# Optimization experiments

Measured on AMD Instinct MI355X. Metric: run time of the kernel, lower is better.

## Reference

```python
import jax, jax.numpy as jnp
import numpy as np

EPS = 1e-5
KEEP_FRAC = 0.925


def conv1x1(x, w, b):
    # x: [B,C,H,W], w: [O,C], b: [O]
    return jnp.einsum('bchw,oc->bohw', x, w) + b[None, :, None, None]


def adain_norm(x):
    m = x.mean(axis=(2, 3), keepdims=True)
    v = x.var(axis=(2, 3), keepdims=True)
    return (x - m) / jnp.sqrt(v + EPS)


def zca_norm(x):
    B, C, H, W = x.shape
    f = x.reshape(B, C, H * W)
    m = f.mean(axis=-1, keepdims=True)
    fc = f - m
    cov = jnp.einsum('bcn,bdn->bcd', fc, fc) / (H * W - 1) + EPS * jnp.eye(C, dtype=x.dtype)
    s, U = jnp.linalg.eigh(cov)
    Ud = U * (1.0 / jnp.sqrt(s + EPS))[:, None, :]          # U @ diag(s^-1/2)
    whiten = jnp.einsum('bce,bde->bcd', Ud, U)              # U diag U^T
    out = jnp.einsum('bcd,bdn->bcn', whiten, fc)
    return out.reshape(B, C, H, W)


def correlation_block(xq, yk, wf, bf, wg, bg):
    B, C, H, W = xq.shape
    f = conv1x1(xq, wf, bf).reshape(B, C, -1)   # [B,C,n_x]
    g = conv1x1(yk, wg, bg).reshape(B, C, -1)   # [B,C,n_y]
    energy = jnp.einsum('bcn,bcm->bnm', f, g)   # f^T g : [B,n_x,n_y]
    corr = jax.nn.softmax(energy, axis=-1)
    atten = corr.mean(axis=1, keepdims=True)    # mean over n_x -> [B,1,n_y]
    return corr, atten


def attn_mask(a):
    # a: [B,1,n]; zero the positions of the k smallest values (union over batch, as in torch)
    n = a.shape[2]
    k = int(n * KEEP_FRAC)
    idx = jnp.argsort(a, axis=2)[:, :, :k]                   # smallest k per (b, channel)
    mask = jnp.ones_like(a).at[:, :, idx.reshape(-1)].set(0.0)
    return mask


def corr_mask(mx, my):
    # mx: [B,1,n_x], my: [B,1,n_y] -> equality mask [B,n_x,n_y]
    return (mx[:, 0, :, None] == my[:, 0, None, :]).astype(mx.dtype)


def savanet_forward(x, y, f_w, f_b, g_w, g_b, sa_f_w, sa_f_b, sa_g_w, sa_g_b, h_w, h_b, out_w, out_b):
    B, C, H, W = x.shape
    n = H * W
    x_adain = adain_norm(x)
    y_adain = adain_norm(y)
    x_zca = zca_norm(x)
    y_zca = zca_norm(y)
    correlation, _ = correlation_block(x_adain, y_adain, f_w, f_b, g_w, g_b)
    _, atten_x = correlation_block(x_zca, x_zca, sa_f_w, sa_f_b, sa_g_w, sa_g_b)
    _, atten_y = correlation_block(y_zca, y_zca, sa_f_w, sa_f_b, sa_g_w, sa_g_b)
    mx = attn_mask(atten_x)
    my = attn_mask(atten_y)
    cmask = corr_mask(mx, my)                               # [B,n,n]
    correlation = cmask * correlation
    l1 = jnp.clip(jnp.abs(correlation).sum(axis=2, keepdims=True), 1e-12, None)
    correlation = correlation / l1                          # F.normalize(p=1, dim=2)
    h = conv1x1(y, h_w, h_b).reshape(B, C, n)               # [B,C,n_y]
    residual = jnp.einsum('bcm,bnm->bcn', h, correlation)   # h @ corr^T -> [B,C,n_x]
    residual = residual.reshape(B, C, H, W)
    residual = conv1x1(residual, out_w, out_b)
    output = x + residual
    return output, atten_x, atten_y


def setup_inputs() -> dict:
    key = jax.random.key(0)
    ks = jax.random.split(key, 10)
    B, C, H, W = 2, 512, 64, 64
    scale = 0.02
    d = {
        'x': jax.random.normal(ks[0], (B, C, H, W), dtype=jnp.float32),
        'y': jax.random.normal(ks[1], (B, C, H, W), dtype=jnp.float32),
        'f_w': jax.random.normal(ks[2], (C, C), dtype=jnp.float32) * scale,
        'f_b': jnp.zeros((C,), dtype=jnp.float32),
        'g_w': jax.random.normal(ks[3], (C, C), dtype=jnp.float32) * scale,
        'g_b': jnp.zeros((C,), dtype=jnp.float32),
        'sa_f_w': jax.random.normal(ks[4], (C, C), dtype=jnp.float32) * scale,
        'sa_f_b': jnp.zeros((C,), dtype=jnp.float32),
        'sa_g_w': jax.random.normal(ks[5], (C, C), dtype=jnp.float32) * scale,
        'sa_g_b': jnp.zeros((C,), dtype=jnp.float32),
        'h_w': jax.random.normal(ks[6], (C, C), dtype=jnp.float32) * scale,
        'h_b': jnp.zeros((C,), dtype=jnp.float32),
        'out_w': jax.random.normal(ks[7], (C, C), dtype=jnp.float32) * scale,
        'out_b': jnp.zeros((C,), dtype=jnp.float32),
    }
    return d


def reference(x, y, f_w, f_b, g_w, g_b, sa_f_w, sa_f_b, sa_g_w, sa_g_b, h_w, h_b, out_w, out_b):
    return savanet_forward(x, y, f_w, f_b, g_w, g_b, sa_f_w, sa_f_b, sa_g_w, sa_g_b, h_w, h_b, out_w, out_b)
```

## Files before the change

### kernel.cpp

```cpp
#include <hip/hip_runtime.h>
#include <cstdint>

static constexpr int B2 = 2;
static constexpr int C = 512;
static constexpr int N = 4096;
static constexpr long CN = (long)C * N;
static constexpr long NC = (long)N * C;
static constexpr long CC = (long)C * C;
static constexpr long NN = (long)N * N;
static constexpr float EPSC = 1e-5f;
static constexpr int KSEL = 308;
static constexpr int NS_ITERS = 4;

typedef __attribute__((ext_vector_type(8))) __bf16 bf16x8;
typedef __attribute__((ext_vector_type(4))) float f32x4;

__device__ __forceinline__ float wredSum(float v){
#pragma unroll
  for (int o = 32; o >= 1; o >>= 1) v += __shfl_xor(v, o, 64);
  return v;
}

__device__ __forceinline__ void gld16(const __bf16* g, __bf16* l){
  __builtin_amdgcn_global_load_lds(
      (const __attribute__((address_space(1))) void*)g,
      (__attribute__((address_space(3))) void*)l, 16, 0, 0);
}

__device__ __forceinline__ void splitw(float v, __bf16* ph, __bf16* pl, long o){
  __bf16 h = (__bf16)v;
  ph[o] = h;
  pl[o] = (__bf16)(v - (float)h);
}

template<int PASSES, int TMH, int OUTMODE, int ROWP>
__global__ __launch_bounds__(256) void k_mm(
    const __bf16* __restrict__ Ah, const __bf16* __restrict__ Al,
    const __bf16* __restrict__ Bh, const __bf16* __restrict__ Bl,
    float* __restrict__ Cf, __bf16* __restrict__ Coh, __bf16* __restrict__ Col,
    int Nn, int K, long sAz, long sBz, long sCz,
    float alpha, const float* __restrict__ alpha_ptr,
    const float* __restrict__ brow, long sBr,
    const float* __restrict__ bcol, long sBc,
    const float* __restrict__ c0p,
    const float* __restrict__ addsrc, long sAddz,
    float* __restrict__ Pm, float* __restrict__ Ps)
{
  constexpr int NB = (PASSES == 3) ? 4 : 2;
  constexpr int SB = (PASSES == 3) ? 2 : 1;
  __shared__ __align__(16) __bf16 sm[NB][128 * 32];
  __shared__ float pmx[2][128], psx[2][128];
  const int z = blockIdx.z;
  const int nwx = gridDim.x;
  int lin = blockIdx.y * nwx + blockIdx.x;
  const int nwg = nwx * gridDim.y;
  if ((nwg & 7) == 0){
    const int cpx = nwg >> 3;
    lin = (lin & 7) * cpx + (lin >> 3);
  }
  const int i0 = (lin % nwx) * 128;
  const int j0 = (lin / nwx) * 128;
  const int tid = threadIdx.x;
  const int lane = tid & 63;
  const int w = tid >> 6;
  const int wr = (w >> 1) * 64, wc = (w & 1) * 64;
  const int lr = lane & 15;
  const int g = lane >> 4;

  const __bf16* pAh = Ah + (long)z * sAz + (long)i0 * K;
  const __bf16* pBh = Bh + (long)z * sBz + (long)j0 * K;
  const __bf16* pAl = (PASSES == 3) ? (Al + (long)z * sAz + (long)i0 * K) : nullptr;
  const __bf16* pBl = (PASSES == 3) ? (Bl + (long)z * sBz + (long)j0 * K) : nullptr;

  f32x4 acc[4][4] = {};

  for (int kt = 0; kt < K; kt += 32){
#pragma unroll
    for (int p = 0; p < 2; ++p){
      const int t2 = p * 256 + tid;
      const int row = t2 >> 2;
      const int gs = (t2 & 3) ^ ((row >> 1) & 3);
      const long go = (long)row * K + kt + gs * 8;
      gld16(pAh + go, &sm[0][t2 * 8]);
      gld16(pBh + go, &sm[SB][t2 * 8]);
      if constexpr (PASSES == 3){
        gld16(pAl + go, &sm[1][t2 * 8]);
        gld16(pBl + go, &sm[3][t2 * 8]);
      }
    }
    __syncthreads();
    bf16x8 fa[4], fal[4], fb[4], fbl[4];
#pragma unroll
    for (int mi = 0; mi < 4; ++mi){
      const int row = wr + mi * 16 + lr;
      const int off = row * 32 + ((g ^ ((row >> 1) & 3)) * 8);
      fa[mi] = *(const bf16x8*)(&sm[0][off]);
      if constexpr (PASSES == 3) fal[mi] = *(const bf16x8*)(&sm[1][off]);
    }
#pragma unroll
    for (int ni = 0; ni < 4; ++ni){
      const int row = wc + ni * 16 + lr;
      const int off = row * 32 + ((g ^ ((row >> 1) & 3)) * 8);
      fb[ni] = *(const bf16x8*)(&sm[SB][off]);
      if constexpr (PASSES == 3) fbl[ni] = *(const bf16x8*)(&sm[3][off]);
    }
#pragma unroll
    for (int mi = 0; mi < 4; ++mi)
#pragma unroll
      for (int ni = 0; ni < 4; ++ni){
        acc[mi][ni] = __builtin_amdgcn_mfma_f32_16x16x32_bf16(fa[mi], fb[ni], acc[mi][ni], 0, 0, 0);
        if constexpr (PASSES == 3){
          acc[mi][ni] = __builtin_amdgcn_mfma_f32_16x16x32_bf16(fa[mi],  fbl[ni], acc[mi][ni], 0, 0, 0);
          acc[mi][ni] = __builtin_amdgcn_mfma_f32_16x16x32_bf16(fal[mi], fb[ni],  acc[mi][ni], 0, 0, 0);
        }
      }
    __syncthreads();
  }

  float al2 = alpha;
  if (alpha_ptr) al2 *= alpha_ptr[z];
  const float c0v = c0p ? c0p[z] : 0.f;
#pragma unroll
  for (int mi = 0; mi < 4; ++mi){
    float mrow[4] = {-3.4e38f, -3.4e38f, -3.4e38f, -3.4e38f};
    float srow[4] = {0.f, 0.f, 0.f, 0.f};
#pragma unroll
    for (int ni = 0; ni < 4; ++ni){
      const int col = j0 + wc + ni * 16 + lr;
      const float bc = (bcol ? bcol[z * sBc + col] : 0.f) + c0v;
#pragma unroll
      for (int j = 0; j < 4; ++j){
        const int row = i0 + wr + mi * 16 + g * 4 + j;
        float v = acc[mi][ni][j] * al2;
        if (TMH) v = (((row == col) ? 3.f : 0.f) - v) * 0.5f;
        if (brow) v += brow[z * sBr + row];
        v += bc;
        if (addsrc) v += addsrc[(long)z * sAddz + (long)row * Nn + col];
        const long o = (long)z * sCz + (long)row * Nn + col;
        if (OUTMODE == 0){ Cf[o] = v; }
        else if (OUTMODE == 1){ __bf16 h = (__bf16)v; Coh[o] = h; Col[o] = (__bf16)(v - (float)h); }
        else { Coh[o] = (__bf16)v; }
        if constexpr (ROWP){
          if (v > mrow[j]){ srow[j] *= __expf(mrow[j] - v); mrow[j] = v; }
          srow[j] += __expf(v - mrow[j]);
        }
      }
    }
    if constexpr (ROWP){
#pragma unroll
      for (int j = 0; j < 4; ++j){
        float m = mrow[j], s = srow[j];
#pragma unroll
        for (int o = 1; o <= 8; o <<= 1){
          const float mo = __shfl_xor(m, o, 64);
          const float so = __shfl_xor(s, o, 64);
          const float nm = fmaxf(m, mo);
          s = s * __expf(m - nm) + so * __expf(mo - nm);
          m = nm;
        }
        if (lr == 0){
          const int rl = wr + mi * 16 + g * 4 + j;
          pmx[w & 1][rl] = m;
          psx[w & 1][rl] = s;
        }
      }
    }
  }
  if constexpr (ROWP){
    __syncthreads();
    if (tid < 128){
      const float m0 = pmx[0][tid], s0 = psx[0][tid];
      const float m1 = pmx[1][tid], s1 = psx[1][tid];
      const float nm = fmaxf(m0, m1);
      const float s = s0 * __expf(m0 - nm) + s1 * __expf(m1 - nm);
      Pm[(long)(j0 >> 7) * N + i0 + tid] = nm;
      Ps[(long)(j0 >> 7) * N + i0 + tid] = s;
    }
  }
}

template<int TMH, int OUTMODE, int NSYZ>
__global__ __launch_bounds__(256) void k_mm64(
    const __bf16* __restrict__ Ah, const __bf16* __restrict__ Al,
    const __bf16* __restrict__ Bh, const __bf16* __restrict__ Bl,
    const __bf16* __restrict__ tH, const __bf16* __restrict__ tL,
    float* __restrict__ Cf, __bf16* __restrict__ Coh, __bf16* __restrict__ Col,
    int Nn, int K, long sAz, long sBz, long sCz, float alpha)
{
  __shared__ __align__(16) __bf16 sm[4][64 * 64];
  const int z = blockIdx.z;
  const __bf16 *bAh, *bAl, *bBh, *bBl;
  long oC;
  if constexpr (NSYZ){
    if (z < 4){
      bAh = Ah + (long)z * CC; bAl = Al + (long)z * CC;
      bBh = tH + (long)z * CC; bBl = tL + (long)z * CC;
      oC = (long)z * CC;
    } else {
      const int zz = z - 4;
      bAh = tH + (long)zz * CC; bAl = tL + (long)zz * CC;
      bBh = Ah + (long)(4 + zz) * CC; bBl = Al + (long)(4 + zz) * CC;
      oC = (long)(4 + zz) * CC;
    }
  } else {
    bAh = Ah + (long)z * sAz; bAl = Al + (long)z * sAz;
    bBh = Bh + (long)z * sBz; bBl = Bl + (long)z * sBz;
    oC = (long)z * sCz;
  }
  const int i0 = blockIdx.x * 64;
  const int j0 = blockIdx.y * 64;
  const int tid = threadIdx.x;
  const int lane = tid & 63;
  const int w = tid >> 6;
  const int wr = (w >> 1) * 32, wc = (w & 1) * 32;
  const int lr = lane & 15;
  const int g = lane >> 4;

  const __bf16* pAh = bAh + (long)i0 * K;
  const __bf16* pAl = bAl + (long)i0 * K;
  const __bf16* pBh = bBh + (long)j0 * K;
  const __bf16* pBl = bBl + (long)j0 * K;

  f32x4 acc[2][2] = {};

  for (int kt = 0; kt < K; kt += 64){
#pragma unroll
    for (int p = 0; p < 2; ++p){
      const int t2 = p * 256 + tid;
      const int row = t2 >> 3;
      const int gs = (t2 & 7) ^ (row & 7);
      const long go = (long)row * K + kt + gs * 8;
      gld16(pAh + go, &sm[0][t2 * 8]);
      gld16(pAl + go, &sm[1][t2 * 8]);
      gld16(pBh + go, &sm[2][t2 * 8]);
      gld16(pBl + go, &sm[3][t2 * 8]);
    }
    __syncthreads();
#pragma unroll
    for (int ks = 0; ks < 2; ++ks){
      bf16x8 fa[2], fal[2], fb[2], fbl[2];
#pragma unroll
      for (int mi = 0; mi < 2; ++mi){
        const int row = wr + mi * 16 + lr;
        const int off = row * 64 + (((ks * 4 + g) ^ (row & 7)) * 8);
        fa[mi]  = *(const bf16x8*)(&sm[0][off]);
        fal[mi] = *(const bf16x8*)(&sm[1][off]);
      }
#pragma unroll
      for (int ni = 0; ni < 2; ++ni){
        const int row = wc + ni * 16 + lr;
        const int off = row * 64 + (((ks * 4 + g) ^ (row & 7)) * 8);
        fb[ni]  = *(const bf16x8*)(&sm[2][off]);
        fbl[ni] = *(const bf16x8*)(&sm[3][off]);
      }
#pragma unroll
      for (int mi = 0; mi < 2; ++mi)
#pragma unroll
        for (int ni = 0; ni < 2; ++ni){
          acc[mi][ni] = __builtin_amdgcn_mfma_f32_16x16x32_bf16(fa[mi],  fb[ni],  acc[mi][ni], 0, 0, 0);
          acc[mi][ni] = __builtin_amdgcn_mfma_f32_16x16x32_bf16(fa[mi],  fbl[ni], acc[mi][ni], 0, 0, 0);
          acc[mi][ni] = __builtin_amdgcn_mfma_f32_16x16x32_bf16(fal[mi], fb[ni],  acc[mi][ni], 0, 0, 0);
        }
    }
    __syncthreads();
  }

#pragma unroll
  for (int mi = 0; mi < 2; ++mi){
#pragma unroll
    for (int ni = 0; ni < 2; ++ni){
      const int col = j0 + wc + ni * 16 + lr;
#pragma unroll
      for (int j = 0; j < 4; ++j){
        const int row = i0 + wr + mi * 16 + g * 4 + j;
        float v = acc[mi][ni][j] * alpha;
        if (TMH) v = (((row == col) ? 3.f : 0.f) - v) * 0.5f;
        const long o = oC + (long)row * Nn + col;
        if (OUTMODE == 0){ Cf[o] = v; }
        else { __bf16 h = (__bf16)v; Coh[o] = h; Col[o] = (__bf16)(v - (float)h); }
      }
    }
  }
}

__global__ __launch_bounds__(256) void k_pv(
    const __bf16* __restrict__ E, const __bf16* __restrict__ Bh,
    const float* __restrict__ rm, const float* __restrict__ rsc,
    const float* __restrict__ mxv, const float* __restrict__ myv,
    __bf16* __restrict__ resH)
{
  __shared__ __align__(16) __bf16 sa[64 * 64];
  __shared__ __align__(16) __bf16 sb[128 * 64];
  const int z = blockIdx.z;
  int lin = blockIdx.y * 64 + blockIdx.x;
  lin = (lin & 7) * 32 + (lin >> 3);
  const int n0 = (lin & 63) * 64;
  const int c0 = (lin >> 6) * 128;
  const int tid = threadIdx.x;
  const int lane = tid & 63;
  const int w = tid >> 6;
  const int wr = (w >> 1) * 32, wc = (w & 1) * 64;
  const int lr = lane & 15, g = lane >> 4;

  const __bf16* pe = E + (long)z * NN + (long)n0 * N;
  const __bf16* pB = Bh + (long)z * CN + (long)c0 * N;

  const int ar = tid >> 2;
  const int slot = tid & 3;
  const float rmv = rm[(long)z * N + n0 + ar];
  const float rsv = rsc[(long)z * N + n0 + ar];
  const float tgt = mxv[n0 + ar];
  const __bf16* per = pe + (long)ar * N;

  f32x4 acc[2][4] = {};

  for (int kt = 0; kt < N; kt += 64){
#pragma unroll
    for (int d = 0; d < 2; ++d){
      const int gd = slot * 2 + d;
      const bf16x8 ev = *(const bf16x8*)(per + kt + gd * 8);
      const float4 m0 = *(const float4*)(myv + kt + gd * 8);
      const float4 m1 = *(const float4*)(myv + kt + gd * 8 + 4);
      bf16x8 pk;
      pk[0] = (__bf16)((m0.x == tgt) ? __expf((float)ev[0] - rmv) * rsv : 0.f);
      pk[1] = (__bf16)((m0.y == tgt) ? __expf((float)ev[1] - rmv) * rsv : 0.f);
      pk[2] = (__bf16)((m0.z == tgt) ? __expf((float)ev[2] - rmv) * rsv : 0.f);
      pk[3] = (__bf16)((m0.w == tgt) ? __expf((float)ev[3] - rmv) * rsv : 0.f);
      pk[4] = (__bf16)((m1.x == tgt) ? __expf((float)ev[4] - rmv) * rsv : 0.f);
      pk[5] = (__bf16)((m1.y == tgt) ? __expf((float)ev[5] - rmv) * rsv : 0.f);
      pk[6] = (__bf16)((m1.z == tgt) ? __expf((float)ev[6] - rmv) * rsv : 0.f);
      pk[7] = (__bf16)((m1.w == tgt) ? __expf((float)ev[7] - rmv) * rsv : 0.f);
      *(bf16x8*)(&sa[ar * 64 + ((gd ^ (ar & 7)) * 8)]) = pk;
    }
#pragma unroll
    for (int p = 0; p < 4; ++p){
      const int t2 = p * 256 + tid;
      const int row = t2 >> 3;
      const int gs = (t2 & 7) ^ (row & 7);
      gld16(pB + (long)row * N + kt + gs * 8, &sb[t2 * 8]);
    }
    __syncthreads();
#pragma unroll
    for (int ks = 0; ks < 2; ++ks){
      bf16x8 fa[2], fb[4];
#pragma unroll
      for (int mi = 0; mi < 2; ++mi){
        const int row = wr + mi * 16 + lr;
        fa[mi] = *(const bf16x8*)(&sa[row * 64 + (((ks * 4 + g) ^ (row & 7)) * 8)]);
      }
#pragma unroll
      for (int ni = 0; ni < 4; ++ni){
        const int row = wc + ni * 16 + lr;
        fb[ni] = *(const bf16x8*)(&sb[row * 64 + (((ks * 4 + g) ^ (row & 7)) * 8)]);
      }
#pragma unroll
      for (int mi = 0; mi < 2; ++mi)
#pragma unroll
        for (int ni = 0; ni < 4; ++ni)
          acc[mi][ni] = __builtin_amdgcn_mfma_f32_16x16x32_bf16(fa[mi], fb[ni], acc[mi][ni], 0, 0, 0);
    }
    __syncthreads();
  }
#pragma unroll
  for (int mi = 0; mi < 2; ++mi)
#pragma unroll
    for (int ni = 0; ni < 4; ++ni){
      const int c = c0 + wc + ni * 16 + lr;
#pragma unroll
      for (int j = 0; j < 4; ++j){
        const int n = n0 + wr + mi * 16 + g * 4 + j;
        resH[(long)z * NC + (long)n * C + c] = (__bf16)acc[mi][ni][j];
      }
    }
}

__global__ __launch_bounds__(256) void k_wtw(const float* __restrict__ A, const float* __restrict__ B,
                                             float* __restrict__ C2, float alpha){
  __shared__ float sa[16][32], sb[16][32];
  const int i0 = blockIdx.x * 32, j0 = blockIdx.y * 32;
  const int t = threadIdx.x;
  const int ti = t & 15, tj = t >> 4;
  const int li = t & 31, lc = t >> 5;
  float acc[2][2] = {};
  for (int cb = 0; cb < C; cb += 16){
    sa[lc][li]     = A[(long)(cb + lc) * C + i0 + li];
    sa[lc + 8][li] = A[(long)(cb + lc + 8) * C + i0 + li];
    sb[lc][li]     = B[(long)(cb + lc) * C + j0 + li];
    sb[lc + 8][li] = B[(long)(cb + lc + 8) * C + j0 + li];
    __syncthreads();
#pragma unroll
    for (int c = 0; c < 16; ++c){
      const float a0 = sa[c][ti * 2], a1 = sa[c][ti * 2 + 1];
      const float b0 = sb[c][tj * 2], b1 = sb[c][tj * 2 + 1];
      acc[0][0] = fmaf(a0, b0, acc[0][0]); acc[0][1] = fmaf(a0, b1, acc[0][1]);
      acc[1][0] = fmaf(a1, b0, acc[1][0]); acc[1][1] = fmaf(a1, b1, acc[1][1]);
    }
    __syncthreads();
  }
#pragma unroll
  for (int r = 0; r < 2; ++r)
#pragma unroll
    for (int s = 0; s < 2; ++s)
      C2[(long)(i0 + ti * 2 + r) * C + j0 + tj * 2 + s] = acc[r][s] * alpha;
}

__global__ __launch_bounds__(256) void k_wtv(const float* __restrict__ W, const float* __restrict__ b,
                                             float* __restrict__ u){
  __shared__ float sb2[C];
  const int t = threadIdx.x;
  sb2[t] = b[t]; sb2[t + 256] = b[t + 256];
  __syncthreads();
  const int e = blockIdx.x * 256 + t;
  float acc = 0.f;
  for (int c = 0; c < C; ++c) acc = fmaf(W[(long)c * C + e], sb2[c], acc);
  u[e] = acc;
}

__global__ void k_dot2(const float* __restrict__ a1, const float* __restrict__ b1,
                       const float* __restrict__ a2, const float* __restrict__ b2,
                       float* __restrict__ c0m2, float* __restrict__ c0s4){
  const int t = threadIdx.x;
  float s1 = 0.f, s2 = 0.f;
  for (int i = t; i < C; i += 256){ s1 += a1[i] * b1[i]; s2 += a2[i] * b2[i]; }
  __shared__ float sh1[4], sh2[4];
  s1 = wredSum(s1); s2 = wredSum(s2);
  if ((t & 63) == 0){ sh1[t >> 6] = s1; sh2[t >> 6] = s2; }
  __syncthreads();
  if (t == 0){
    float d1 = sh1[0] + sh1[1] + sh1[2] + sh1[3];
    float d2 = sh2[0] + sh2[1] + sh2[2] + sh2[3];
    c0m2[0] = d1; c0m2[1] = d1;
    c0s4[0] = d2; c0s4[1] = d2; c0s4[2] = d2; c0s4[3] = d2;
  }
}

__global__ __launch_bounds__(256) void k_pixvec(const __bf16* __restrict__ X, const float* __restrict__ u,
                                                float* __restrict__ out){
  const int z = blockIdx.y;
  const int wv = threadIdx.x >> 6, lane = threadIdx.x & 63;
  const int n = blockIdx.x * 4 + wv;
  float acc = 0.f;
  for (int d = lane; d < C; d += 64) acc += (float)X[(long)z * NC + (long)n * C + d] * u[d];
  acc = wredSum(acc);
  if (lane == 0) out[(long)z * N + n] = acc;
}

__global__ __launch_bounds__(256) void k_stats(const float* __restrict__ x, const float* __restrict__ y,
                                               float* __restrict__ meanv, float* __restrict__ invs){
  const int bid = blockIdx.x;
  const int t = bid >> 9, c = bid & 511;
  const float* src = (t < 2 ? x : y) + (long)(t & 1) * CN + (long)c * N;
  const int tid = threadIdx.x;
  float s1 = 0.f, s2 = 0.f;
  for (int i = tid; i < N; i += 256){ float v = src[i]; s1 += v; s2 += v * v; }
  __shared__ float sh1[4], sh2[4];
  s1 = wredSum(s1); s2 = wredSum(s2);
  if ((tid & 63) == 0){ sh1[tid >> 6] = s1; sh2[tid >> 6] = s2; }
  __syncthreads();
  if (tid == 0){
    float m = (sh1[0] + sh1[1] + sh1[2] + sh1[3]) * (1.f / (float)N);
    float ex2 = (sh2[0] + sh2[1] + sh2[2] + sh2[3]) * (1.f / (float)N);
    float var = ex2 - m * m;
    meanv[t * C + c] = m;
    invs[t * C + c] = rsqrtf((var > 0.f ? var : 0.f) + EPSC);
  }
}

__global__ __launch_bounds__(256) void k_prep(const float* __restrict__ src,
                                              const float* __restrict__ meanv, const float* __restrict__ invs, int toff,
                                              __bf16* __restrict__ adH,
                                              __bf16* __restrict__ fcH, __bf16* __restrict__ fcL,
                                              __bf16* __restrict__ ccH, __bf16* __restrict__ ccL,
                                              __bf16* __restrict__ rwH){
  __shared__ float tile[64][65];
  const int z = blockIdx.z;
  const int n0 = blockIdx.x * 64;
  const int c0 = blockIdx.y * 64;
  const int tid = threadIdx.x;
  const int tx = tid & 63, ty = tid >> 6;
  const int tgt = toff + z;
#pragma unroll
  for (int it = 0; it < 16; ++it){
    const int cc = it * 4 + ty;
    const float v = src[(long)z * CN + (long)(c0 + cc) * N + n0 + tx];
    tile[cc][tx] = v;
    const float cen = v - meanv[tgt * C + c0 + cc];
    splitw(cen, ccH, ccL, (long)tgt * CN + (long)(c0 + cc) * N + n0 + tx);
  }
  __syncthreads();
  const float m = meanv[tgt * C + c0 + tx];
  const float r = invs[tgt * C + c0 + tx];
#pragma unroll
  for (int it = 0; it < 16; ++it){
    const int p = it * 4 + ty;
    const float v = tile[tx][p];
    const float cen = v - m;
    const long o = (long)z * NC + (long)(n0 + p) * C + c0 + tx;
    adH[o] = (__bf16)(cen * r);
    splitw(cen, fcH, fcL, (long)tgt * NC + (long)(n0 + p) * C + c0 + tx);
    if (rwH) rwH[o] = (__bf16)v;
  }
}

__global__ __launch_bounds__(256) void k_wcvt(const float* __restrict__ s, __bf16* __restrict__ h,
                                              __bf16* __restrict__ l, int n){
  int i = blockIdx.x * 256 + threadIdx.x;
  if (i < n) splitw(s[i], h, l, i);
}
__global__ __launch_bounds__(256) void k_wcvt_h(const float* __restrict__ s, __bf16* __restrict__ h, int n){
  int i = blockIdx.x * 256 + threadIdx.x;
  if (i < n) h[i] = (__bf16)s[i];
}

__global__ void k_diag(float* __restrict__ cov){
  const int z = blockIdx.x, t = threadIdx.x;
  for (int i = t; i < C; i += 256) cov[(long)z * CC + (long)i * C + i] += 2.f * EPSC;
}

__global__ __launch_bounds__(256) void k_powit(const float* __restrict__ cov,
                                               float* __restrict__ invt, float* __restrict__ invsqt){
  __shared__ float v[C], red[4];
  const int z = blockIdx.x, t = threadIdx.x;
  const float* A = cov + (long)z * CC;
  const int j0 = t, j1 = t + 256;
  v[j0] = 1.f + 0.0003f * (float)j0;
  v[j1] = 1.f + 0.0003f * (float)j1;
  __syncthreads();
  float lam = 1.f;
  for (int it = 0; it < 4; ++it){
    float w0a = 0.f, w0b = 0.f, w1a = 0.f, w1b = 0.f;
#pragma unroll 8
    for (int c = 0; c < C; c += 2){
      const float vc0 = v[c], vc1 = v[c + 1];
      w0a = fmaf(A[(long)c * C + j0], vc0, w0a);
      w1a = fmaf(A[(long)c * C + j1], vc0, w1a);
      w0b = fmaf(A[(long)(c + 1) * C + j0], vc1, w0b);
      w1b = fmaf(A[(long)(c + 1) * C + j1], vc1, w1b);
    }
    const float w0 = w0a + w0b, w1 = w1a + w1b;
    float s = w0 * w0 + w1 * w1;
    s = wredSum(s);
    if ((t & 63) == 0) red[t >> 6] = s;
    __syncthreads();
    const float nrm = sqrtf(red[0] + red[1] + red[2] + red[3]);
    lam = nrm;
    const float inv = 1.f / nrm;
    v[j0] = w0 * inv;
    v[j1] = w1 * inv;
    __syncthreads();
  }
  if (t == 0){
    const float tt = 1.02f * lam;
    invt[z] = 1.f / tt;
    invsqt[z] = rsqrtf(tt);
  }
}

__global__ __launch_bounds__(256) void k_ns_init(const float* __restrict__ cov, const float* __restrict__ invt,
                                                 __bf16* __restrict__ h, __bf16* __restrict__ l,
                                                 __bf16* __restrict__ cph, __bf16* __restrict__ cpl){
  const int r = blockIdx.x, z = blockIdx.y;
  const long base = (long)z * CC + (long)r * C;
  const float it = invt[z];
  for (int i = threadIdx.x; i < C; i += 256){
    const float v = cov[base + i] * it;
    splitw(v, h, l, base + i);
    splitw(v, cph, cpl, base + i);
    h[4 * CC + base + i] = (__bf16)((i == r) ? 1.f : 0.f);
    l[4 * CC + base + i] = (__bf16)0.f;
  }
}

__global__ __launch_bounds__(256) void k_prowmerge(const float* __restrict__ Pm, const float* __restrict__ Ps,
                                                   float* __restrict__ rm, float* __restrict__ rsc){
  const int row = blockIdx.x * 256 + threadIdx.x;
  float m = -3.4e38f, s = 0.f;
#pragma unroll 4
  for (int p = 0; p < 32; ++p){
    const float mp = Pm[(long)p * N + row];
    const float sp = Ps[(long)p * N + row];
    const float nm = fmaxf(m, mp);
    s = s * __expf(m - nm) + sp * __expf(mp - nm);
    m = nm;
  }
  rm[row] = m;
  rsc[row] = 1.f / s;
}

__global__ __launch_bounds__(256) void k_colaccum(const float* __restrict__ E, const float* __restrict__ rowmax,
                                                  const float* __restrict__ rowscale, float* __restrict__ partials){
  const int j = (blockIdx.x * 256 + threadIdx.x) * 4;
  const int r0 = blockIdx.y * 128;
  float4 acc = {0.f, 0.f, 0.f, 0.f};
  for (int r2 = r0; r2 < r0 + 128; ++r2){
    const float4 e = *reinterpret_cast<const float4*>(E + (long)r2 * N + j);
    const float rmv = rowmax[r2], rsv = rowscale[r2];
    acc.x += __expf(e.x - rmv) * rsv;
    acc.y += __expf(e.y - rmv) * rsv;
    acc.z += __expf(e.z - rmv) * rsv;
    acc.w += __expf(e.w - rmv) * rsv;
  }
  *reinterpret_cast<float4*>(partials + (long)blockIdx.y * N + j) = acc;
}

__global__ __launch_bounds__(256) void k_colreduce(const float* __restrict__ partials, float* __restrict__ att){
  const int j = blockIdx.x * 256 + threadIdx.x;
  float s = 0.f;
#pragma unroll 4
  for (int p = 0; p < 32; ++p) s += partials[(long)p * N + j];
  att[j] = s * (1.f / (float)N);
}

__global__ __launch_bounds__(256) void k_rowstats1(
    const __bf16* __restrict__ E, const float* __restrict__ mx, const float* __restrict__ my,
    float* __restrict__ rowmax, float* __restrict__ rowscale)
{
  const int zz = blockIdx.y;
  const int r0 = blockIdx.x * 16;
  const int tid = threadIdx.x;
  const int rr = tid >> 4;
  const int l16 = tid & 15;
  const int row = r0 + rr;
  const __bf16* pe = E + (long)zz * NN + (long)row * N;
  const float target = mx[row];
  float m = -3.4e38f, s = 0.f, sm = 0.f;
  for (int i = l16 * 8; i < N; i += 128){
    const bf16x8 ev = *(const bf16x8*)(pe + i);
    const float4 w0 = *(const float4*)(my + i);
    const float4 w1 = *(const float4*)(my + i + 4);
    float e[8];
#pragma unroll
    for (int k = 0; k < 8; ++k) e[k] = (float)ev[k];
    float mv = fmaxf(fmaxf(fmaxf(e[0], e[1]), fmaxf(e[2], e[3])),
                     fmaxf(fmaxf(e[4], e[5]), fmaxf(e[6], e[7])));
    if (mv > m){ const float sc = __expf(m - mv); s *= sc; sm *= sc; m = mv; }
    float x0 = __expf(e[0] - m), x1 = __expf(e[1] - m), x2 = __expf(e[2] - m), x3 = __expf(e[3] - m);
    float x4 = __expf(e[4] - m), x5 = __expf(e[5] - m), x6 = __expf(e[6] - m), x7 = __expf(e[7] - m);
    s += ((x0 + x1) + (x2 + x3)) + ((x4 + x5) + (x6 + x7));
    if (w0.x == target) sm += x0;
    if (w0.y == target) sm += x1;
    if (w0.z == target) sm += x2;
    if (w0.w == target) sm += x3;
    if (w1.x == target) sm += x4;
    if (w1.y == target) sm += x5;
    if (w1.z == target) sm += x6;
    if (w1.w == target) sm += x7;
  }
#pragma unroll
  for (int o = 8; o >= 1; o >>= 1){
    const float mo = __shfl_xor(m, o, 64);
    const float so = __shfl_xor(s, o, 64);
    const float smo = __shfl_xor(sm, o, 64);
    const float nm = fmaxf(m, mo);
    const float sc0 = __expf(m - nm), sc1 = __expf(mo - nm);
    s = s * sc0 + so * sc1;
    sm = sm * sc0 + smo * sc1;
    m = nm;
  }
  if (l16 == 0){
    float l1 = sm / s;
    if (l1 < 1e-12f) l1 = 1e-12f;
    rowscale[(long)zz * N + row] = 1.f / (s * l1);
    rowmax[(long)zz * N + row] = m;
  }
}

__global__ __launch_bounds__(256) void k_radix(const float* __restrict__ a, float* __restrict__ thr){
  __shared__ unsigned int vals[N];
  __shared__ float shc[4];
  __shared__ unsigned int p_sh;
  __shared__ int k_sh;
  const float* pa = a + (long)blockIdx.x * N;
  const int tid = threadIdx.x;
  for (int i = tid; i < N; i += 256) vals[i] = __float_as_uint(pa[i]);
  if (tid == 0){ p_sh = 0u; k_sh = KSEL; }
  __syncthreads();
  for (int b = 31; b >= 0; --b){
    const unsigned int bit = 1u << b;
    const unsigned int above = (b == 31) ? 0u : ~((bit << 1) - 1u);
    const unsigned int p = p_sh;
    int cnt = 0;
    for (int i = tid; i < N; i += 256){
      unsigned int v = vals[i];
      if ((v & above) == p && (v & bit)) cnt++;
    }
    float cf = wredSum((float)cnt);
    if ((tid & 63) == 0) shc[tid >> 6] = cf;
    __syncthreads();
    if (tid == 0){
      int c1 = (int)(shc[0] + shc[1] + shc[2] + shc[3] + 0.5f);
      if (k_sh <= c1) p_sh = p | bit;
      else k_sh -= c1;
    }
    __syncthreads();
  }
  if (tid == 0) thr[blockIdx.x] = __uint_as_float(p_sh);
}

__global__ __launch_bounds__(256) void k_mask(const float* __restrict__ ax, const float* __restrict__ ay,
                                              const float* __restrict__ thr, float* __restrict__ mx,
                                              float* __restrict__ my){
  int j = blockIdx.x * 256 + threadIdx.x;
  mx[j] = (ax[j] >= thr[0] && ax[N + j] >= thr[1]) ? 1.f : 0.f;
  my[j] = (ay[j] >= thr[2] && ay[N + j] >= thr[3]) ? 1.f : 0.f;
}

extern "C" void kernel_launch(void* const* d_in, const int* in_sizes, int n_in,
                              void* d_out, int out_size, void* d_ws, size_t ws_size,
                              hipStream_t stream)
{
  const float* x     = (const float*)d_in[0];
  const float* y     = (const float*)d_in[1];
  const float* f_w   = (const float*)d_in[2];
  const float* f_b   = (const float*)d_in[3];
  const float* g_w   = (const float*)d_in[4];
  const float* g_b   = (const float*)d_in[5];
  const float* saf_w = (const float*)d_in[6];
  const float* saf_b = (const float*)d_in[7];
  const float* sag_w = (const float*)d_in[8];
  const float* sag_b = (const float*)d_in[9];
  const float* h_w   = (const float*)d_in[10];
  const float* h_b   = (const float*)d_in[11];
  const float* ow    = (const float*)d_in[12];
  const float* ob    = (const float*)d_in[13];

  const size_t MBy = 1ull << 20;
  char* base = (char*)d_ws;
  if (ws_size < 206 * MBy) return;
  auto F  = [&](size_t off){ return (float*)(base + off); };
  auto Bp = [&](size_t off){ return (__bf16*)(base + off); };

  float *E0 = F(0);
  __bf16 *Ebf = Bp(0);
  __bf16 *ccH = Bp(0), *ccL = Bp(16*MBy);
  float  *covb = F(32*MBy);
  __bf16 *zpolH = Bp(36*MBy), *zpolL = Bp(38*MBy);
  __bf16 *covPH = Bp(40*MBy), *covPL = Bp(42*MBy);
  float  *KsTf = F(44*MBy), *K2tf = F(45*MBy);
  __bf16 *KsTH = Bp(46*MBy), *KsTL = Bp(46*MBy + 512*1024);
  __bf16 *K2tH = Bp(47*MBy), *hwH = Bp(47*MBy + 512*1024);
  __bf16 *tpH = Bp(48*MBy), *tpL = Bp(50*MBy);
  __bf16 *xaH = Bp(64*MBy);
  __bf16 *xzH = Bp(64*MBy), *xzL = Bp(80*MBy);
  __bf16 *ypmH = Bp(96*MBy);
  __bf16 *AsH = Bp(96*MBy), *AsL = Bp(112*MBy);
  __bf16 *fcH = Bp(128*MBy), *fcL = Bp(144*MBy);
  __bf16 *resH = Bp(128*MBy);
  __bf16 *nsAh = Bp(160*MBy), *nsAl = Bp(164*MBy);
  __bf16 *nsBh = Bp(168*MBy), *nsBl = Bp(172*MBy);
  __bf16 *A2H = Bp(176*MBy);
  __bf16 *yaH = Bp(184*MBy);
  __bf16 *hH  = Bp(192*MBy);
  __bf16 *owH = Bp(200*MBy);
  size_t so = 200 * MBy + 512 * 1024;
  auto SF = [&](size_t bytes){ float* p = F(so); so += bytes; return p; };
  float *meanv = SF(8*1024), *invs = SF(8*1024);
  float *rm = SF(32*1024), *rsc = SF(32*1024);
  float *mxv = SF(16*1024), *myv = SF(16*1024);
  float *rvec2 = SF(32*1024), *cvec2 = SF(32*1024);
  float *rvS = SF(64*1024), *cvS = SF(64*1024);
  float *u1m = SF(2*1024), *u2m = SF(2*1024), *u1s = SF(2*1024), *u2s = SF(2*1024);
  float *c0m2 = SF(64), *c0s4 = SF(64), *thr = SF(64);
  float *invt = SF(64), *invsqt = SF(64);
  float *partials = F(201*MBy);
  float *Pm = F(201*MBy + 512*1024);
  float *Ps = F(201*MBy + 1024*1024);

  float* outm = (float*)d_out;
  float* attx = outm + B2 * CN;
  float* atty = attx + (long)B2 * N;

  k_stats<<<dim3(4 * C), dim3(256), 0, stream>>>(x, y, meanv, invs);
  k_prep<<<dim3(64, 8, 2), dim3(256), 0, stream>>>(x, meanv, invs, 0, xaH, fcH, fcL, ccH, ccL, nullptr);
  k_prep<<<dim3(64, 8, 2), dim3(256), 0, stream>>>(y, meanv, invs, 2, yaH, fcH, fcL, ccH, ccL, ypmH);

  k_wtw<<<dim3(16, 16), dim3(256), 0, stream>>>(sag_w, saf_w, KsTf, 1.f);
  k_wtw<<<dim3(16, 16), dim3(256), 0, stream>>>(g_w, f_w, K2tf, 1.f);
  {
    const int nb = (int)(CC / 256);
    k_wcvt<<<nb, 256, 0, stream>>>(KsTf, KsTH, KsTL, (int)CC);
    k_wcvt_h<<<nb, 256, 0, stream>>>(K2tf, K2tH, (int)CC);
    k_wcvt_h<<<nb, 256, 0, stream>>>(h_w, hwH, (int)CC);
    k_wcvt_h<<<nb, 256, 0, stream>>>(ow, owH, (int)CC);
  }
  k_wtv<<<dim3(2), dim3(256), 0, stream>>>(g_w, f_b, u1m);
  k_wtv<<<dim3(2), dim3(256), 0, stream>>>(f_w, g_b, u2m);
  k_wtv<<<dim3(2), dim3(256), 0, stream>>>(sag_w, saf_b, u1s);
  k_wtv<<<dim3(2), dim3(256), 0, stream>>>(saf_w, sag_b, u2s);
  k_dot2<<<dim3(1), dim3(256), 0, stream>>>(f_b, g_b, saf_b, sag_b, c0m2, c0s4);
  k_pixvec<<<dim3(N / 4, 2), dim3(256), 0, stream>>>(xaH, u2m, rvec2);
  k_pixvec<<<dim3(N / 4, 2), dim3(256), 0, stream>>>(yaH, u1m, cvec2);

  k_mm64<0,0,0><<<dim3(8, 8, 4), dim3(256), 0, stream>>>(
      ccH, ccL, ccH, ccL, nullptr, nullptr, covb, nullptr, nullptr, C, N, CN, CN, CC, 1.f / (float)(N - 1));
  k_diag<<<dim3(4), dim3(256), 0, stream>>>(covb);
  k_powit<<<dim3(4), dim3(256), 0, stream>>>(covb, invt, invsqt);

  k_mm<1,0,2,0><<<dim3(32, 4, 2), dim3(256), 0, stream>>>(xaH, nullptr, K2tH, nullptr, nullptr, A2H, nullptr,
      C, C, NC, 0, NC, 1.f, nullptr, nullptr, 0, nullptr, 0, nullptr, nullptr, 0, nullptr, nullptr);
  k_mm<1,0,2,0><<<dim3(4, 32, 2), dim3(256), 0, stream>>>(hwH, nullptr, ypmH, nullptr, nullptr, hH, nullptr,
      N, C, 0, NC, CN, 1.f, nullptr, h_b, 0, nullptr, 0, nullptr, nullptr, 0, nullptr, nullptr);

  k_ns_init<<<dim3(C, 4), dim3(256), 0, stream>>>(covb, invt, nsAh, nsAl, covPH, covPL);
  __bf16 *cah = nsAh, *cal = nsAl, *cbh = nsBh, *cbl = nsBl;
  for (int it = 0; it < NS_ITERS; ++it){
    k_mm64<1,1,0><<<dim3(8, 8, 4), dim3(256), 0, stream>>>(
        cah + 4*CC, cal + 4*CC, cah, cal, nullptr, nullptr, nullptr, tpH, tpL, C, C, CC, CC, CC, 1.f);
    k_mm64<0,1,1><<<dim3(8, 8, 8), dim3(256), 0, stream>>>(
        cah, cal, nullptr, nullptr, tpH, tpL, nullptr, cbh, cbl, C, C, CC, CC, CC, 1.f);
    __bf16* t;
    t = cah; cah = cbh; cbh = t;
    t = cal; cal = cbl; cbl = t;
  }
  k_mm64<0,1,0><<<dim3(8, 8, 4), dim3(256), 0, stream>>>(
      cah + 4*CC, cal + 4*CC, cah + 4*CC, cal + 4*CC, nullptr, nullptr, nullptr, tpH, tpL, C, C, CC, CC, CC, 1.f);
  k_mm64<1,1,0><<<dim3(8, 8, 4), dim3(256), 0, stream>>>(
      covPH, covPL, tpH, tpL, nullptr, nullptr, nullptr, cbh, cbl, C, C, CC, CC, CC, 1.f);
  k_mm64<0,1,0><<<dim3(8, 8, 4), dim3(256), 0, stream>>>(
      cah + 4*CC, cal + 4*CC, cbh, cbl, nullptr, nullptr, nullptr, zpolH, zpolL, C, C, CC, CC, CC, 1.f);

  k_mm<3,0,1,0><<<dim3(32, 4, 4), dim3(256), 0, stream>>>(fcH, fcL, zpolH, zpolL, nullptr, xzH, xzL,
      C, C, NC, CC, NC, 1.f, invsqt, nullptr, 0, nullptr, 0, nullptr, nullptr, 0, nullptr, nullptr);

  k_pixvec<<<dim3(N / 4, 4), dim3(256), 0, stream>>>(xzH, u2s, rvS);
  k_pixvec<<<dim3(N / 4, 4), dim3(256), 0, stream>>>(xzH, u1s, cvS);
  k_mm<3,0,1,0><<<dim3(32, 4, 4), dim3(256), 0, stream>>>(xzH, xzL, KsTH, KsTL, nullptr, AsH, AsL,
      C, C, NC, 0, NC, 1.f, nullptr, nullptr, 0, nullptr, 0, nullptr, nullptr, 0, nullptr, nullptr);

  for (int z = 0; z < 4; ++z){
    k_mm<3,0,0,1><<<dim3(32, 32, 1), dim3(256), 0, stream>>>(AsH + (long)z*NC, AsL + (long)z*NC,
        xzH + (long)z*NC, xzL + (long)z*NC, E0, nullptr, nullptr,
        N, C, 0, 0, 0, 1.f, nullptr, rvS + (long)z*N, 0, cvS + (long)z*N, 0, c0s4, nullptr, 0, Pm, Ps);
    k_prowmerge<<<dim3(16), dim3(256), 0, stream>>>(Pm, Ps, rm, rsc);
    k_colaccum<<<dim3(4, 32), dim3(256), 0, stream>>>(E0, rm, rsc, partials);
    k_colreduce<<<dim3(16), dim3(256), 0, stream>>>(partials, (z < 2 ? attx : atty) + (long)(z & 1) * N);
  }

  k_radix<<<dim3(2), dim3(256), 0, stream>>>(attx, thr);
  k_radix<<<dim3(2), dim3(256), 0, stream>>>(atty, thr + 2);
  k_mask<<<dim3(16), dim3(256), 0, stream>>>(attx, atty, thr, mxv, myv);

  k_mm<1,0,2,0><<<dim3(32, 32, 2), dim3(256), 0, stream>>>(A2H, nullptr, yaH, nullptr, nullptr, Ebf, nullptr,
      N, C, NC, NC, NN, 1.f, nullptr, rvec2, N, cvec2, N, c0m2, nullptr, 0, nullptr, nullptr);
  k_rowstats1<<<dim3(N / 16, 2), dim3(256), 0, stream>>>(Ebf, mxv, myv, rm, rsc);
  k_pv<<<dim3(64, 4, 2), dim3(256), 0, stream>>>(Ebf, hH, rm, rsc, mxv, myv, resH);
  k_mm<1,0,0,0><<<dim3(4, 32, 2), dim3(256), 0, stream>>>(owH, nullptr, resH, nullptr, outm, nullptr, nullptr,
      N, C, 0, NC, CN, 1.f, nullptr, ob, 0, nullptr, 0, nullptr, x, CN, nullptr, nullptr);
}
```

Measured before the change: 1.272 ms.

## Replace 3-pass split-bf16 GEMMs with single-pass K=1536 concatenated hi/lo layout

Stores the zca-whitened activations, the self-attention weight and the projected activations in a concatenated [hi|lo|hi] or [hi|hi|lo] layout along K (width 1536). The 3-pass split-precision matmuls then become single-pass bf16 GEMMs over K=1536, and a leading-dimension parameter is added to the GEMM output. This is meant to remove the multi-pass B-tile loading and bookkeeping in the big N×N energy GEMMs while keeping the three cross terms. The cost is a larger workspace footprint, more bytes read per K, and a workspace layout that had to be reshuffled.

```diff
diff --git a/kernel.cpp b/kernel.cpp
--- a/kernel.cpp
+++ b/kernel.cpp
@@ -8,6 +8,7 @@
 static constexpr long NC = (long)N * C;
 static constexpr long CC = (long)C * C;
 static constexpr long NN = (long)N * N;
+static constexpr long NL = (long)N * 1536;
 static constexpr float EPSC = 1e-5f;
 static constexpr int KSEL = 308;
 static constexpr int NS_ITERS = 4;
@@ -38,7 +39,7 @@
     const __bf16* __restrict__ Ah, const __bf16* __restrict__ Al,
     const __bf16* __restrict__ Bh, const __bf16* __restrict__ Bl,
     float* __restrict__ Cf, __bf16* __restrict__ Coh, __bf16* __restrict__ Col,
-    int Nn, int K, long sAz, long sBz, long sCz,
+    int Nn, int K, int ldC, long sAz, long sBz, long sCz,
     float alpha, const float* __restrict__ alpha_ptr,
     const float* __restrict__ brow, long sBr,
     const float* __restrict__ bcol, long sBc,
@@ -136,10 +137,12 @@
         if (brow) v += brow[z * sBr + row];
         v += bc;
         if (addsrc) v += addsrc[(long)z * sAddz + (long)row * Nn + col];
-        const long o = (long)z * sCz + (long)row * Nn + col;
+        const long o = (long)z * sCz + (long)row * ldC + col;
         if (OUTMODE == 0){ Cf[o] = v; }
         else if (OUTMODE == 1){ __bf16 h = (__bf16)v; Coh[o] = h; Col[o] = (__bf16)(v - (float)h); }
-        else { Coh[o] = (__bf16)v; }
+        else if (OUTMODE == 2){ Coh[o] = (__bf16)v; }
+        else if (OUTMODE == 3){ __bf16 h = (__bf16)v; Coh[o] = h; Coh[o + 512] = (__bf16)(v - (float)h); Coh[o + 1024] = h; }
+        else { __bf16 h = (__bf16)v; Coh[o] = h; Coh[o + 512] = h; Coh[o + 1024] = (__bf16)(v - (float)h); }
         if constexpr (ROWP){
           if (v > mrow[j]){ srow[j] *= __expf(mrow[j] - v); mrow[j] = v; }
           srow[j] += __expf(v - mrow[j]);
@@ -435,12 +438,12 @@
 }
 
 __global__ __launch_bounds__(256) void k_pixvec(const __bf16* __restrict__ X, const float* __restrict__ u,
-                                                float* __restrict__ out){
+                                                float* __restrict__ out, long sz, int ld){
   const int z = blockIdx.y;
   const int wv = threadIdx.x >> 6, lane = threadIdx.x & 63;
   const int n = blockIdx.x * 4 + wv;
   float acc = 0.f;
-  for (int d = lane; d < C; d += 64) acc += (float)X[(long)z * NC + (long)n * C + d] * u[d];
+  for (int d = lane; d < C; d += 64) acc += (float)X[(long)z * sz + (long)n * ld + d] * u[d];
   acc = wredSum(acc);
   if (lane == 0) out[(long)z * N + n] = acc;
 }
@@ -502,14 +505,22 @@
   }
 }
 
-__global__ __launch_bounds__(256) void k_wcvt(const float* __restrict__ s, __bf16* __restrict__ h,
-                                              __bf16* __restrict__ l, int n){
-  int i = blockIdx.x * 256 + threadIdx.x;
-  if (i < n) splitw(s[i], h, l, i);
-}
 __global__ __launch_bounds__(256) void k_wcvt_h(const float* __restrict__ s, __bf16* __restrict__ h, int n){
   int i = blockIdx.x * 256 + threadIdx.x;
   if (i < n) h[i] = (__bf16)s[i];
+}
+
+__global__ __launch_bounds__(256) void k_wcvt3(const float* __restrict__ s, __bf16* __restrict__ o3){
+  const int i = blockIdx.x * 256 + threadIdx.x;
+  if (i < (int)CC){
+    const int r = i >> 9, c = i & 511;
+    const float v = s[i];
+    const __bf16 h = (__bf16)v;
+    const long base = (long)r * 1536 + c;
+    o3[base] = h;
+    o3[base + 512] = h;
+    o3[base + 1024] = (__bf16)(v - (float)h);
+  }
 }
 
 __global__ void k_diag(float* __restrict__ cov){
@@ -725,6 +736,7 @@
   const float* ob    = (const float*)d_in[13];
 
   const size_t MBy = 1ull << 20;
+  const size_t KBy = 1ull << 10;
   char* base = (char*)d_ws;
   if (ws_size < 206 * MBy) return;
   auto F  = [&](size_t off){ return (float*)(base + off); };
@@ -737,34 +749,35 @@
   __bf16 *zpolH = Bp(36*MBy), *zpolL = Bp(38*MBy);
   __bf16 *covPH = Bp(40*MBy), *covPL = Bp(42*MBy);
   float  *KsTf = F(44*MBy), *K2tf = F(45*MBy);
-  __bf16 *KsTH = Bp(46*MBy), *KsTL = Bp(46*MBy + 512*1024);
-  __bf16 *K2tH = Bp(47*MBy), *hwH = Bp(47*MBy + 512*1024);
-  __bf16 *tpH = Bp(48*MBy), *tpL = Bp(50*MBy);
+  __bf16 *Ks3 = Bp(46*MBy);
+  __bf16 *K2tH = Bp(47*MBy + 512*KBy);
+  __bf16 *hwH = Bp(48*MBy);
+  __bf16 *tpH = Bp(48*MBy + 512*KBy), *tpL = Bp(50*MBy + 512*KBy);
   __bf16 *xaH = Bp(64*MBy);
-  __bf16 *xzH = Bp(64*MBy), *xzL = Bp(80*MBy);
-  __bf16 *ypmH = Bp(96*MBy);
-  __bf16 *AsH = Bp(96*MBy), *AsL = Bp(112*MBy);
-  __bf16 *fcH = Bp(128*MBy), *fcL = Bp(144*MBy);
-  __bf16 *resH = Bp(128*MBy);
+  __bf16 *xz3 = Bp(64*MBy);
+  __bf16 *ypmH = Bp(112*MBy);
+  __bf16 *fcH = Bp(120*MBy), *fcL = Bp(136*MBy);
+  __bf16 *As3 = Bp(112*MBy);
+  __bf16 *resH = Bp(152*MBy);
   __bf16 *nsAh = Bp(160*MBy), *nsAl = Bp(164*MBy);
   __bf16 *nsBh = Bp(168*MBy), *nsBl = Bp(172*MBy);
   __bf16 *A2H = Bp(176*MBy);
   __bf16 *yaH = Bp(184*MBy);
   __bf16 *hH  = Bp(192*MBy);
   __bf16 *owH = Bp(200*MBy);
-  size_t so = 200 * MBy + 512 * 1024;
+  size_t so = 200 * MBy + 512 * KBy;
   auto SF = [&](size_t bytes){ float* p = F(so); so += bytes; return p; };
-  float *meanv = SF(8*1024), *invs = SF(8*1024);
-  float *rm = SF(32*1024), *rsc = SF(32*1024);
-  float *mxv = SF(16*1024), *myv = SF(16*1024);
-  float *rvec2 = SF(32*1024), *cvec2 = SF(32*1024);
-  float *rvS = SF(64*1024), *cvS = SF(64*1024);
-  float *u1m = SF(2*1024), *u2m = SF(2*1024), *u1s = SF(2*1024), *u2s = SF(2*1024);
+  float *meanv = SF(8*KBy), *invs = SF(8*KBy);
+  float *rm = SF(32*KBy), *rsc = SF(32*KBy);
+  float *mxv = SF(16*KBy), *myv = SF(16*KBy);
+  float *rvec2 = SF(32*KBy), *cvec2 = SF(32*KBy);
+  float *rvS = SF(64*KBy), *cvS = SF(64*KBy);
+  float *u1m = SF(2*KBy), *u2m = SF(2*KBy), *u1s = SF(2*KBy), *u2s = SF(2*KBy);
   float *c0m2 = SF(64), *c0s4 = SF(64), *thr = SF(64);
   float *invt = SF(64), *invsqt = SF(64);
   float *partials = F(201*MBy);
-  float *Pm = F(201*MBy + 512*1024);
-  float *Ps = F(201*MBy + 1024*1024);
+  float *Pm = F(201*MBy + 512*KBy);
+  float *Ps = F(202*MBy);
 
   float* outm = (float*)d_out;
   float* attx = outm + B2 * CN;
@@ -778,7 +791,7 @@
   k_wtw<<<dim3(16, 16), dim3(256), 0, stream>>>(g_w, f_w, K2tf, 1.f);
   {
     const int nb = (int)(CC / 256);
-    k_wcvt<<<nb, 256, 0, stream>>>(KsTf, KsTH, KsTL, (int)CC);
+    k_wcvt3<<<nb, 256, 0, stream>>>(KsTf, Ks3);
     k_wcvt_h<<<nb, 256, 0, stream>>>(K2tf, K2tH, (int)CC);
     k_wcvt_h<<<nb, 256, 0, stream>>>(h_w, hwH, (int)CC);
     k_wcvt_h<<<nb, 256, 0, stream>>>(ow, owH, (int)CC);
@@ -788,8 +801,8 @@
   k_wtv<<<dim3(2), dim3(256), 0, stream>>>(sag_w, saf_b, u1s);
   k_wtv<<<dim3(2), dim3(256), 0, stream>>>(saf_w, sag_b, u2s);
   k_dot2<<<dim3(1), dim3(256), 0, stream>>>(f_b, g_b, saf_b, sag_b, c0m2, c0s4);
-  k_pixvec<<<dim3(N / 4, 2), dim3(256), 0, stream>>>(xaH, u2m, rvec2);
-  k_pixvec<<<dim3(N / 4, 2), dim3(256), 0, stream>>>(yaH, u1m, cvec2);
+  k_pixvec<<<dim3(N / 4, 2), dim3(256), 0, stream>>>(xaH, u2m, rvec2, NC, C);
+  k_pixvec<<<dim3(N / 4, 2), dim3(256), 0, stream>>>(yaH, u1m, cvec2, NC, C);
 
   k_mm64<0,0,0><<<dim3(8, 8, 4), dim3(256), 0, stream>>>(
       ccH, ccL, ccH, ccL, nullptr, nullptr, covb, nullptr, nullptr, C, N, CN, CN, CC, 1.f / (float)(N - 1));
@@ -797,9 +810,9 @@
   k_powit<<<dim3(4), dim3(256), 0, stream>>>(covb, invt, invsqt);
 
   k_mm<1,0,2,0><<<dim3(32, 4, 2), dim3(256), 0, stream>>>(xaH, nullptr, K2tH, nullptr, nullptr, A2H, nullptr,
-      C, C, NC, 0, NC, 1.f, nullptr, nullptr, 0, nullptr, 0, nullptr, nullptr, 0, nullptr, nullptr);
+      C, C, C, NC, 0, NC, 1.f, nullptr, nullptr, 0, nullptr, 0, nullptr, nullptr, 0, nullptr, nullptr);
   k_mm<1,0,2,0><<<dim3(4, 32, 2), dim3(256), 0, stream>>>(hwH, nullptr, ypmH, nullptr, nullptr, hH, nullptr,
-      N, C, 0, NC, CN, 1.f, nullptr, h_b, 0, nullptr, 0, nullptr, nullptr, 0, nullptr, nullptr);
+      N, C, N, 0, NC, CN, 1.f, nullptr, h_b, 0, nullptr, 0, nullptr, nullptr, 0, nullptr, nullptr);
 
   k_ns_init<<<dim3(C, 4), dim3(256), 0, stream>>>(covb, invt, nsAh, nsAl, covPH, covPL);
   __bf16 *cah = nsAh, *cal = nsAl, *cbh = nsBh, *cbl = nsBl;
@@ -819,18 +832,18 @@
   k_mm64<0,1,0><<<dim3(8, 8, 4), dim3(256), 0, stream>>>(
       cah + 4*CC, cal + 4*CC, cbh, cbl, nullptr, nullptr, nullptr, zpolH, zpolL, C, C, CC, CC, CC, 1.f);
 
-  k_mm<3,0,1,0><<<dim3(32, 4, 4), dim3(256), 0, stream>>>(fcH, fcL, zpolH, zpolL, nullptr, xzH, xzL,
-      C, C, NC, CC, NC, 1.f, invsqt, nullptr, 0, nullptr, 0, nullptr, nullptr, 0, nullptr, nullptr);
-
-  k_pixvec<<<dim3(N / 4, 4), dim3(256), 0, stream>>>(xzH, u2s, rvS);
-  k_pixvec<<<dim3(N / 4, 4), dim3(256), 0, stream>>>(xzH, u1s, cvS);
-  k_mm<3,0,1,0><<<dim3(32, 4, 4), dim3(256), 0, stream>>>(xzH, xzL, KsTH, KsTL, nullptr, AsH, AsL,
-      C, C, NC, 0, NC, 1.f, nullptr, nullptr, 0, nullptr, 0, nullptr, nullptr, 0, nullptr, nullptr);
+  k_mm<3,0,3,0><<<dim3(32, 4, 4), dim3(256), 0, stream>>>(fcH, fcL, zpolH, zpolL, nullptr, xz3, nullptr,
+      C, C, 1536, NC, CC, NL, 1.f, invsqt, nullptr, 0, nullptr, 0, nullptr, nullptr, 0, nullptr, nullptr);
+
+  k_pixvec<<<dim3(N / 4, 4), dim3(256), 0, stream>>>(xz3, u2s, rvS, NL, 1536);
+  k_pixvec<<<dim3(N / 4, 4), dim3(256), 0, stream>>>(xz3, u1s, cvS, NL, 1536);
+  k_mm<1,0,4,0><<<dim3(32, 4, 4), dim3(256), 0, stream>>>(xz3, nullptr, Ks3, nullptr, nullptr, As3, nullptr,
+      C, 1536, 1536, NL, 0, NL, 1.f, nullptr, nullptr, 0, nullptr, 0, nullptr, nullptr, 0, nullptr, nullptr);
 
   for (int z = 0; z < 4; ++z){
-    k_mm<3,0,0,1><<<dim3(32, 32, 1), dim3(256), 0, stream>>>(AsH + (long)z*NC, AsL + (long)z*NC,
-        xzH + (long)z*NC, xzL + (long)z*NC, E0, nullptr, nullptr,
-        N, C, 0, 0, 0, 1.f, nullptr, rvS + (long)z*N, 0, cvS + (long)z*N, 0, c0s4, nullptr, 0, Pm, Ps);
+    k_mm<1,0,0,1><<<dim3(32, 32, 1), dim3(256), 0, stream>>>(As3 + (long)z*NL, nullptr,
+        xz3 + (long)z*NL, nullptr, E0, nullptr, nullptr,
+        N, 1536, N, 0, 0, 0, 1.f, nullptr, rvS + (long)z*N, 0, cvS + (long)z*N, 0, c0s4, nullptr, 0, Pm, Ps);
     k_prowmerge<<<dim3(16), dim3(256), 0, stream>>>(Pm, Ps, rm, rsc);
     k_colaccum<<<dim3(4, 32), dim3(256), 0, stream>>>(E0, rm, rsc, partials);
     k_colreduce<<<dim3(16), dim3(256), 0, stream>>>(partials, (z < 2 ? attx : atty) + (long)(z & 1) * N);
@@ -841,9 +854,9 @@
   k_mask<<<dim3(16), dim3(256), 0, stream>>>(attx, atty, thr, mxv, myv);
 
   k_mm<1,0,2,0><<<dim3(32, 32, 2), dim3(256), 0, stream>>>(A2H, nullptr, yaH, nullptr, nullptr, Ebf, nullptr,
-      N, C, NC, NC, NN, 1.f, nullptr, rvec2, N, cvec2, N, c0m2, nullptr, 0, nullptr, nullptr);
+      N, C, N, NC, NC, NN, 1.f, nullptr, rvec2, N, cvec2, N, c0m2, nullptr, 0, nullptr, nullptr);
   k_rowstats1<<<dim3(N / 16, 2), dim3(256), 0, stream>>>(Ebf, mxv, myv, rm, rsc);
   k_pv<<<dim3(64, 4, 2), dim3(256), 0, stream>>>(Ebf, hH, rm, rsc, mxv, myv, resH);
   k_mm<1,0,0,0><<<dim3(4, 32, 2), dim3(256), 0, stream>>>(owH, nullptr, resH, nullptr, outm, nullptr, nullptr,
-      N, C, 0, NC, CN, 1.f, nullptr, ob, 0, nullptr, 0, nullptr, x, CN, nullptr, nullptr);
-}
+      N, C, N, 0, NC, CN, 1.f, nullptr, ob, 0, nullptr, 0, nullptr, x, CN, nullptr, nullptr);
+}
```

New measurement: 1.420 ms. 1.12x slower.
